# Performance work log

Measured on AMD Instinct MI355X. Metric: run time of the kernel, lower is better.

The kernel has to match this reference:

```python
import jax, jax.numpy as jnp
import numpy as np

EMBED_DIM = 1024
N_HEAD = 16
HEAD_DIM = EMBED_DIM // N_HEAD


def setup_inputs() -> dict:
    key = jax.random.key(0)
    k1, k2, k3 = jax.random.split(key, 3)
    B, S = 2, 2048
    x = jax.random.normal(k1, (B, S, EMBED_DIM), dtype=jnp.float32)
    # kaiming-style scale for the packed QKV projection and output projection
    w_qkv = jax.random.normal(k2, (3 * EMBED_DIM, EMBED_DIM), dtype=jnp.float32) * np.sqrt(2.0 / EMBED_DIM)
    w0 = jax.random.normal(k3, (EMBED_DIM, EMBED_DIM), dtype=jnp.float32) * np.sqrt(2.0 / EMBED_DIM)
    return {"x": x, "w_qkv": w_qkv, "w0": w0}


def reference(x, w_qkv, w0):
    B, S, E = x.shape
    # fused QKV projection (Linear with no bias): x @ w_qkv.T -> [B,S,3E]
    qkv = jnp.einsum('bse,fe->bsf', x, w_qkv)
    q, k, v = jnp.split(qkv, 3, axis=-1)
    # reshape to [B, H, S, D]
    def heads(t):
        return t.reshape(B, S, N_HEAD, HEAD_DIM).transpose(0, 2, 1, 3)
    q, k, v = heads(q), heads(k), heads(v)
    scale = 1.0 / np.sqrt(HEAD_DIM).astype(np.float32)
    scores = jnp.einsum('bhsd,bhtd->bhst', q, k) * scale  # [B,H,S,S]
    # causal additive bias: -inf above the diagonal (same math as the precomputed bias tensor)
    causal = jnp.tril(jnp.ones((S, S), dtype=bool))
    scores = jnp.where(causal, scores, -jnp.inf)
    probs = jax.nn.softmax(scores, axis=-1)
    e = jnp.einsum('bhst,bhtd->bhsd', probs, v)  # [B,H,S,D]
    e = e.transpose(0, 2, 1, 3).reshape(B, S, E)
    # output projection: E @ w0.T
    return jnp.einsum('bse,fe->bsf', e, w0)
```

## Files before the change

### kernel.cpp

```cpp
#include <hip/hip_runtime.h>


typedef unsigned short u16;
typedef short bf16x8 __attribute__((ext_vector_type(8)));
typedef float f32x4 __attribute__((ext_vector_type(4)));
typedef unsigned short u16x4 __attribute__((ext_vector_type(4)));

#define S_LEN 2048
#define EMB 1024
#define NH 16
#define HD 64
#define QKV_W 3072
#define BATCH 2
#define CSC 0.18033688f

static __device__ __forceinline__ u16 f2bf(float f) {
    unsigned x = __float_as_uint(f);
    return (u16)((x + 0x7fffu + ((x >> 16) & 1u)) >> 16);
}

static __device__ __forceinline__ void gld_lds16(const u16* g, u16* l) {
    __builtin_amdgcn_global_load_lds(
        (const __attribute__((address_space(1))) void*)g,
        (__attribute__((address_space(3))) void*)l, 16, 0, 0);
}

#define XN4 (BATCH * S_LEN * EMB / 4)
#define WQ4 (QKV_W * EMB / 4)
#define W04 (EMB * EMB / 4)
__global__ __launch_bounds__(256) void cvt_all(const float* __restrict__ x,
                                               const float* __restrict__ wq,
                                               const float* __restrict__ w0,
                                               u16* __restrict__ xb,
                                               u16* __restrict__ wqb,
                                               u16* __restrict__ w0b) {
    int i = blockIdx.x * 256 + threadIdx.x;
    const float* src;
    u16* dst;
    int off;
    if (i < XN4) { src = x; dst = xb; off = i; }
    else if (i < XN4 + WQ4) { src = wq; dst = wqb; off = i - XN4; }
    else { src = w0; dst = w0b; off = i - XN4 - WQ4; }
    float4 v = ((const float4*)src)[off];
    u16x4 o;
    o[0] = f2bf(v.x); o[1] = f2bf(v.y); o[2] = f2bf(v.z); o[3] = f2bf(v.w);
    ((u16x4*)dst)[off] = o;
}

template <typename OutT, int BN>
__global__ __launch_bounds__(256) void gemm_bt(const u16* __restrict__ A,
                                               const u16* __restrict__ Bt,
                                               OutT* __restrict__ C,
                                               int M, int N, int K, int qcols) {
    constexpr int NF = BN / 32;
    __shared__ alignas(16) u16 As[128 * 32];
    __shared__ alignas(16) u16 Bs[BN * 32];
    const int tid = threadIdx.x;
    const int wave = tid >> 6, lane = tid & 63;
    const int quad = lane >> 4, lr = lane & 15;
    const int m0 = blockIdx.y * 128, n0 = blockIdx.x * BN;
    const int wm = (wave & 1) * 64, wn = (wave >> 1) * (BN / 2);
    const float sc = (n0 < qcols) ? CSC : 1.0f;

    f32x4 acc[4][NF] = {};

    for (int k0 = 0; k0 < K; k0 += 32) {
#pragma unroll
        for (int i = 0; i < 2; ++i) {
            int chunk = tid + i * 256;
            int row = chunk >> 2;
            int col8 = (chunk & 3) * 8;
            gld_lds16(&A[(size_t)(m0 + row) * K + k0 + col8], &As[row * 32 + col8]);
        }
#pragma unroll
        for (int i = 0; i < BN / 64; ++i) {
            int chunk = tid + i * 256;
            int row = chunk >> 2;
            int col8 = (chunk & 3) * 8;
            gld_lds16(&Bt[(size_t)(n0 + row) * K + k0 + col8], &Bs[row * 32 + col8]);
        }
        __syncthreads();
        bf16x8 af[4], bf[NF];
#pragma unroll
        for (int i = 0; i < 4; ++i)
            af[i] = *(const bf16x8*)&As[(wm + i * 16 + lr) * 32 + quad * 8];
#pragma unroll
        for (int i = 0; i < NF; ++i)
            bf[i] = *(const bf16x8*)&Bs[(wn + i * 16 + lr) * 32 + quad * 8];
#pragma unroll
        for (int mi = 0; mi < 4; ++mi)
#pragma unroll
            for (int ni = 0; ni < NF; ++ni)
                acc[mi][ni] = __builtin_amdgcn_mfma_f32_16x16x32_bf16(
                    af[mi], bf[ni], acc[mi][ni], 0, 0, 0);
        __syncthreads();
    }

#pragma unroll
    for (int mi = 0; mi < 4; ++mi) {
#pragma unroll
        for (int r = 0; r < 4; ++r) {
            int gr = m0 + wm + mi * 16 + quad * 4 + r;
#pragma unroll
            for (int ni = 0; ni < NF; ++ni) {
                int gc = n0 + wn + ni * 16 + lr;
                float v = acc[mi][ni][r] * sc;
                if constexpr (sizeof(OutT) == 2)
                    C[(size_t)gr * N + gc] = (OutT)f2bf(v);
                else
                    C[(size_t)gr * N + gc] = (OutT)v;
            }
        }
    }
}

__global__ __launch_bounds__(256) void transpose_v(const u16* __restrict__ qkv,
                                                   u16* __restrict__ vt) {
    __shared__ alignas(16) u16 t[64][72];
    const int s0 = blockIdx.x * 64;
    const int bh = blockIdx.y;
    const int b = bh >> 4, h = bh & 15;
#pragma unroll
    for (int i = 0; i < 2; ++i) {
        int chunk = threadIdx.x + i * 256;
        int row = chunk >> 3;
        int c8 = (chunk & 7) * 8;
        uint4 v = *(const uint4*)&qkv[(size_t)(b * S_LEN + s0 + row) * QKV_W +
                                      2 * EMB + h * HD + c8];
        const u16* p = (const u16*)&v;
#pragma unroll
        for (int jj = 0; jj < 8; ++jj) t[c8 + jj][row] = p[jj];
    }
    __syncthreads();
#pragma unroll
    for (int i = 0; i < 2; ++i) {
        int chunk = threadIdx.x + i * 256;
        int d = chunk >> 3;
        int c8 = (chunk & 7) * 8;
        uint4 v = *(const uint4*)&t[d][c8];
        *(uint4*)&vt[((size_t)bh * HD + d) * S_LEN + s0 + c8] = v;
    }
}

__global__ __launch_bounds__(512, 4) void attn(const u16* __restrict__ qkv,
                                               const u16* __restrict__ vt,
                                               u16* __restrict__ e) {
    const int tid = threadIdx.x;
    const int w = tid >> 6, lane = tid & 63;
    const int quad = lane >> 4, lr = lane & 15;
    const int wq = w & 3, hv = w >> 2;
    const int tA = blockIdx.y;
    const int tB = 31 - tA;
    const int bh = blockIdx.x, b = bh >> 4, h = bh & 15;

    __shared__ alignas(16) u16 smem[17408];
    u16* Ks = smem;
    u16* Vs = smem + 8192;

    const u16* qkv_b = qkv + (size_t)b * S_LEN * QKV_W;
    const u16* qrowA = qkv_b + (size_t)(tA * 64 + wq * 16 + lr) * QKV_W + h * HD + quad * 8;
    const u16* qrowB = qkv_b + (size_t)(tB * 64 + wq * 16 + lr) * QKV_W + h * HD + quad * 8;
    const bf16x8 qfA0 = *(const bf16x8*)(qrowA);
    const bf16x8 qfA1 = *(const bf16x8*)(qrowA + 32);
    const bf16x8 qfB0 = *(const bf16x8*)(qrowB);
    const bf16x8 qfB1 = *(const bf16x8*)(qrowB + 32);

    const u16* kbase = qkv_b + EMB + h * HD;
    const u16* vbase = vt + (size_t)bh * HD * S_LEN;

    f32x4 oA[4] = {}, oB[4] = {};
    float lsA = 0.f, lsB = 0.f;
    const int qgA = tA * 64 + wq * 16 + lr;
    const int qgB = tB * 64 + wq * 16 + lr;

    const int sr = wq * 16 + (lane >> 2);
    const int scl = (lane & 3) * 8;
    const int scg = ((lane & 3) ^ ((lane >> 3) & 3)) * 8;

    auto stage = [&](int j, int bb) {
        const int kv0 = j * 64;
        if (w < 4) {
            gld_lds16(kbase + (size_t)(kv0 + sr) * QKV_W + scg,
                      &Ks[bb * 4096 + sr * 32 + scl]);
            gld_lds16(kbase + (size_t)(kv0 + sr) * QKV_W + 32 + scg,
                      &Ks[bb * 4096 + 2048 + sr * 32 + scl]);
        } else {
            gld_lds16(vbase + (size_t)sr * S_LEN + kv0 + scg,
                      &Vs[bb * 4096 + sr * 32 + scl]);
            gld_lds16(vbase + (size_t)sr * S_LEN + kv0 + 32 + scg,
                      &Vs[bb * 4096 + 2048 + sr * 32 + scl]);
        }
    };

    const int xq8 = (quad ^ ((lr >> 1) & 3)) * 8;

    auto softpack = [&](const f32x4* s, bool diag, int qg, int kvg,
                        float& lsum) -> bf16x8 {
        float p[8];
#pragma unroll
        for (int nt = 0; nt < 2; ++nt)
#pragma unroll
            for (int r = 0; r < 4; ++r) {
                float pv = exp2f(s[nt][r]);
                if (diag) pv = (kvg + nt * 16 + quad * 4 + r > qg) ? 0.f : pv;
                p[nt * 4 + r] = pv;
            }
        lsum += ((p[0] + p[1]) + (p[2] + p[3])) + ((p[4] + p[5]) + (p[6] + p[7]));
        unsigned x0 = __builtin_amdgcn_perm(__float_as_uint(p[1]),
                                            __float_as_uint(p[0]), 0x07060302u);
        unsigned x1 = __builtin_amdgcn_perm(__float_as_uint(p[3]),
                                            __float_as_uint(p[2]), 0x07060302u);
        unsigned x2 = __builtin_amdgcn_perm(__float_as_uint(p[5]),
                                            __float_as_uint(p[4]), 0x07060302u);
        unsigned x3 = __builtin_amdgcn_perm(__float_as_uint(p[7]),
                                            __float_as_uint(p[6]), 0x07060302u);
        asm("v_permlane32_swap_b32 %0, %1" : "+v"(x0), "+v"(x2));
        asm("v_permlane16_swap_b32 %0, %1" : "+v"(x0), "+v"(x2));
        asm("v_permlane32_swap_b32 %0, %1" : "+v"(x1), "+v"(x3));
        asm("v_permlane16_swap_b32 %0, %1" : "+v"(x1), "+v"(x3));
        union { unsigned u[4]; bf16x8 v; } r;
        r.u[0] = x0; r.u[1] = x1; r.u[2] = x2; r.u[3] = x3;
        return r.v;
    };

    stage(0, 0);
    for (int j = 0; j <= tB; ++j) {
        const int bb = j & 1;
        __syncthreads();
        if (j < tB) stage(j + 1, 1 - bb);
        const bool doA = (j <= tA);
        const u16* ks = &Ks[bb * 4096];
        const u16* vs = &Vs[bb * 4096];
        const int kvh = hv * 32;

        f32x4 sB[2], sA[2];
#pragma unroll
        for (int nt = 0; nt < 2; ++nt) {
            const int kvr = kvh + nt * 16 + lr;
            bf16x8 k0 = *(const bf16x8*)&ks[kvr * 32 + xq8];
            bf16x8 k1 = *(const bf16x8*)&ks[2048 + kvr * 32 + xq8];
            f32x4 z = {};
            z = __builtin_amdgcn_mfma_f32_16x16x32_bf16(k0, qfB0, z, 0, 0, 0);
            z = __builtin_amdgcn_mfma_f32_16x16x32_bf16(k1, qfB1, z, 0, 0, 0);
            sB[nt] = z;
            if (doA) {
                f32x4 za = {};
                za = __builtin_amdgcn_mfma_f32_16x16x32_bf16(k0, qfA0, za, 0, 0, 0);
                za = __builtin_amdgcn_mfma_f32_16x16x32_bf16(k1, qfA1, za, 0, 0, 0);
                sA[nt] = za;
            }
        }

        const int kvg = j * 64 + kvh;
        const bf16x8 pB = softpack(sB, j == tB, qgB, kvg, lsB);
        bf16x8 pA = {};
        if (doA) pA = softpack(sA, j == tA, qgA, kvg, lsA);

#pragma unroll
        for (int nt = 0; nt < 4; ++nt) {
            bf16x8 v = *(const bf16x8*)&vs[hv * 2048 + (nt * 16 + lr) * 32 + xq8];
            oB[nt] = __builtin_amdgcn_mfma_f32_16x16x32_bf16(pB, v, oB[nt], 0, 0, 0);
            if (doA) oA[nt] = __builtin_amdgcn_mfma_f32_16x16x32_bf16(pA, v, oA[nt], 0, 0, 0);
        }
    }

    float lfA = lsA + __shfl_xor(lsA, 16, 64);
    lfA += __shfl_xor(lfA, 32, 64);
    float lfB = lsB + __shfl_xor(lsB, 16, 64);
    lfB += __shfl_xor(lfB, 32, 64);
    __syncthreads();
    float* mA = (float*)smem;
    float* mB = mA + 64 * 66;
    float* lAr = mB + 64 * 66;
    float* lBr = lAr + 64;
    if (hv) {
#pragma unroll
        for (int nt = 0; nt < 4; ++nt)
#pragma unroll
            for (int r = 0; r < 4; ++r)
                mA[(wq * 16 + quad * 4 + r) * 66 + nt * 16 + lr] = oA[nt][r];
        if (lane < 16) lAr[wq * 16 + lane] = lfA;
    } else {
#pragma unroll
        for (int nt = 0; nt < 4; ++nt)
#pragma unroll
            for (int r = 0; r < 4; ++r)
                mB[(wq * 16 + quad * 4 + r) * 66 + nt * 16 + lr] = oB[nt][r];
        if (lane < 16) lBr[wq * 16 + lane] = lfB;
    }
    __syncthreads();
    if (!hv) {
        float lff = lfA + lAr[wq * 16 + lr];
#pragma unroll
        for (int r = 0; r < 4; ++r) {
            float inv = 1.0f / __shfl(lff, quad * 4 + r, 64);
            size_t row = (size_t)(b * S_LEN + tA * 64 + wq * 16 + quad * 4 + r) * EMB + h * HD;
#pragma unroll
            for (int nt = 0; nt < 4; ++nt)
                e[row + nt * 16 + lr] =
                    f2bf((oA[nt][r] + mA[(wq * 16 + quad * 4 + r) * 66 + nt * 16 + lr]) * inv);
        }
    } else {
        float lff = lfB + lBr[wq * 16 + lr];
#pragma unroll
        for (int r = 0; r < 4; ++r) {
            float inv = 1.0f / __shfl(lff, quad * 4 + r, 64);
            size_t row = (size_t)(b * S_LEN + tB * 64 + wq * 16 + quad * 4 + r) * EMB + h * HD;
#pragma unroll
            for (int nt = 0; nt < 4; ++nt)
                e[row + nt * 16 + lr] =
                    f2bf((oB[nt][r] + mB[(wq * 16 + quad * 4 + r) * 66 + nt * 16 + lr]) * inv);
        }
    }
}

extern "C" void kernel_launch(void* const* d_in, const int* in_sizes, int n_in,
                              void* d_out, int out_size, void* d_ws, size_t ws_size,
                              hipStream_t stream) {
    const float* x = (const float*)d_in[0];
    const float* w_qkv = (const float*)d_in[1];
    const float* w0 = (const float*)d_in[2];
    float* out = (float*)d_out;

    const size_t M = (size_t)BATCH * S_LEN;
    u16* xb = (u16*)d_ws;
    u16* wqb = xb + M * EMB;
    u16* w0b = wqb + (size_t)QKV_W * EMB;
    u16* qkvb = w0b + (size_t)EMB * EMB;
    u16* vtb = qkvb + M * QKV_W;
    u16* eb = vtb + (size_t)BATCH * NH * HD * S_LEN;

    cvt_all<<<(XN4 + WQ4 + W04) / 256, 256, 0, stream>>>(x, w_qkv, w0, xb, wqb, w0b);

    gemm_bt<u16, 128><<<dim3(QKV_W / 128, M / 128), 256, 0, stream>>>(
        xb, wqb, qkvb, (int)M, QKV_W, EMB, EMB);

    transpose_v<<<dim3(S_LEN / 64, BATCH * NH), 256, 0, stream>>>(qkvb, vtb);

    attn<<<dim3(BATCH * NH, 16), 512, 0, stream>>>(qkvb, vtb, eb);

    gemm_bt<float, 64><<<dim3(EMB / 64, M / 128), 256, 0, stream>>>(
        eb, w0b, out, (int)M, EMB, EMB, 0);
}
```

Measured before the change: 183.7 us.

## Load K and V fragments directly from global into registers, dropping LDS staging

Replaces the double-buffered global-to-LDS staging of K and V tiles (with __syncthreads per KV block) by per-wave direct global loads into MFMA operand registers. K fragments for the next block are prefetched into alternating register sets, and V is loaded after the QK MFMAs so the load overlaps the softmax. It also adds s_setprio around the MFMA sections. This removes the LDS traffic and block barriers, but each wave now fetches its own K/V from global/L2 with no sharing across the four query waves, and global load latency is exposed on a shorter timeline.

```diff
diff --git a/kernel.cpp b/kernel.cpp
--- a/kernel.cpp
+++ b/kernel.cpp
@@ -154,8 +154,6 @@
     const int bh = blockIdx.x, b = bh >> 4, h = bh & 15;
 
     __shared__ alignas(16) u16 smem[17408];
-    u16* Ks = smem;
-    u16* Vs = smem + 8192;
 
     const u16* qkv_b = qkv + (size_t)b * S_LEN * QKV_W;
     const u16* qrowA = qkv_b + (size_t)(tA * 64 + wq * 16 + lr) * QKV_W + h * HD + quad * 8;
@@ -165,34 +163,29 @@
     const bf16x8 qfB0 = *(const bf16x8*)(qrowB);
     const bf16x8 qfB1 = *(const bf16x8*)(qrowB + 32);
 
-    const u16* kbase = qkv_b + EMB + h * HD;
-    const u16* vbase = vt + (size_t)bh * HD * S_LEN;
+    const int kvh = hv * 32;
+    const u16* kbase = qkv_b + EMB + h * HD + (size_t)(kvh + lr) * QKV_W + quad * 8;
+    const u16* vbase = vt + (size_t)bh * HD * S_LEN + (size_t)lr * S_LEN + kvh + quad * 8;
 
     f32x4 oA[4] = {}, oB[4] = {};
     float lsA = 0.f, lsB = 0.f;
     const int qgA = tA * 64 + wq * 16 + lr;
     const int qgB = tB * 64 + wq * 16 + lr;
 
-    const int sr = wq * 16 + (lane >> 2);
-    const int scl = (lane & 3) * 8;
-    const int scg = ((lane & 3) ^ ((lane >> 3) & 3)) * 8;
-
-    auto stage = [&](int j, int bb) {
-        const int kv0 = j * 64;
-        if (w < 4) {
-            gld_lds16(kbase + (size_t)(kv0 + sr) * QKV_W + scg,
-                      &Ks[bb * 4096 + sr * 32 + scl]);
-            gld_lds16(kbase + (size_t)(kv0 + sr) * QKV_W + 32 + scg,
-                      &Ks[bb * 4096 + 2048 + sr * 32 + scl]);
-        } else {
-            gld_lds16(vbase + (size_t)sr * S_LEN + kv0 + scg,
-                      &Vs[bb * 4096 + sr * 32 + scl]);
-            gld_lds16(vbase + (size_t)sr * S_LEN + kv0 + 32 + scg,
-                      &Vs[bb * 4096 + 2048 + sr * 32 + scl]);
+    auto loadK = [&](int j, bf16x8 (&kf)[4]) {
+        const u16* kp = kbase + (size_t)j * 64 * QKV_W;
+#pragma unroll
+        for (int nt = 0; nt < 2; ++nt) {
+            kf[2 * nt]     = *(const bf16x8*)(kp + (size_t)nt * 16 * QKV_W);
+            kf[2 * nt + 1] = *(const bf16x8*)(kp + (size_t)nt * 16 * QKV_W + 32);
         }
     };
-
-    const int xq8 = (quad ^ ((lr >> 1) & 3)) * 8;
+    auto loadV = [&](int j, bf16x8 (&vf)[4]) {
+        const u16* vp = vbase + j * 64;
+#pragma unroll
+        for (int nt = 0; nt < 4; ++nt)
+            vf[nt] = *(const bf16x8*)(vp + (size_t)nt * 16 * S_LEN);
+    };
 
     auto softpack = [&](const f32x4* s, bool diag, int qg, int kvg,
                         float& lsum) -> bf16x8 {
@@ -223,45 +216,47 @@
         return r.v;
     };
 
-    stage(0, 0);
-    for (int j = 0; j <= tB; ++j) {
-        const int bb = j & 1;
-        __syncthreads();
-        if (j < tB) stage(j + 1, 1 - bb);
+    auto iterate = [&](int j, bf16x8 (&kv)[4]) {
         const bool doA = (j <= tA);
-        const u16* ks = &Ks[bb * 4096];
-        const u16* vs = &Vs[bb * 4096];
-        const int kvh = hv * 32;
-
         f32x4 sB[2], sA[2];
+        __builtin_amdgcn_s_setprio(1);
 #pragma unroll
         for (int nt = 0; nt < 2; ++nt) {
-            const int kvr = kvh + nt * 16 + lr;
-            bf16x8 k0 = *(const bf16x8*)&ks[kvr * 32 + xq8];
-            bf16x8 k1 = *(const bf16x8*)&ks[2048 + kvr * 32 + xq8];
             f32x4 z = {};
-            z = __builtin_amdgcn_mfma_f32_16x16x32_bf16(k0, qfB0, z, 0, 0, 0);
-            z = __builtin_amdgcn_mfma_f32_16x16x32_bf16(k1, qfB1, z, 0, 0, 0);
+            z = __builtin_amdgcn_mfma_f32_16x16x32_bf16(kv[2 * nt], qfB0, z, 0, 0, 0);
+            z = __builtin_amdgcn_mfma_f32_16x16x32_bf16(kv[2 * nt + 1], qfB1, z, 0, 0, 0);
             sB[nt] = z;
             if (doA) {
                 f32x4 za = {};
-                za = __builtin_amdgcn_mfma_f32_16x16x32_bf16(k0, qfA0, za, 0, 0, 0);
-                za = __builtin_amdgcn_mfma_f32_16x16x32_bf16(k1, qfA1, za, 0, 0, 0);
+                za = __builtin_amdgcn_mfma_f32_16x16x32_bf16(kv[2 * nt], qfA0, za, 0, 0, 0);
+                za = __builtin_amdgcn_mfma_f32_16x16x32_bf16(kv[2 * nt + 1], qfA1, za, 0, 0, 0);
                 sA[nt] = za;
             }
         }
-
+        __builtin_amdgcn_s_setprio(0);
+        loadV(j, kv);
         const int kvg = j * 64 + kvh;
         const bf16x8 pB = softpack(sB, j == tB, qgB, kvg, lsB);
         bf16x8 pA = {};
         if (doA) pA = softpack(sA, j == tA, qgA, kvg, lsA);
-
+        __builtin_amdgcn_s_setprio(1);
 #pragma unroll
         for (int nt = 0; nt < 4; ++nt) {
-            bf16x8 v = *(const bf16x8*)&vs[hv * 2048 + (nt * 16 + lr) * 32 + xq8];
-            oB[nt] = __builtin_amdgcn_mfma_f32_16x16x32_bf16(pB, v, oB[nt], 0, 0, 0);
-            if (doA) oA[nt] = __builtin_amdgcn_mfma_f32_16x16x32_bf16(pA, v, oA[nt], 0, 0, 0);
-        }
+            oB[nt] = __builtin_amdgcn_mfma_f32_16x16x32_bf16(pB, kv[nt], oB[nt], 0, 0, 0);
+            if (doA)
+                oA[nt] = __builtin_amdgcn_mfma_f32_16x16x32_bf16(pA, kv[nt], oA[nt], 0, 0, 0);
+        }
+        __builtin_amdgcn_s_setprio(0);
+    };
+
+    bf16x8 kvX[4], kvY[4];
+    loadK(0, kvX);
+    for (int j = 0; j <= tB; j += 2) {
+        if (j < tB) loadK(j + 1, kvY);
+        iterate(j, kvX);
+        if (j + 1 > tB) break;
+        if (j + 1 < tB) loadK(j + 2, kvX);
+        iterate(j + 1, kvY);
     }
 
     float lfA = lsA + __shfl_xor(lsA, 16, 64);
```

Result: slower. 245.7 us (+33.7%).

## Halve attention block to 4 waves, each computing two 16-row query fragments

Applied to the files above, without the earlier changes.

The attention kernel now uses 256 threads (4 waves) instead of 512. Each wave handles two 16-row query fragments, so every K and V fragment read from LDS feeds twice as many MFMAs. All four waves now stage both K and V tiles, and the tile-pair order across blockIdx.y is permuted so that long and short causal work interleaves. The cost is higher register use per wave (launch bounds drop to 2 blocks) and fewer waves available to hide latency.

```diff
diff --git a/kernel.cpp b/kernel.cpp
--- a/kernel.cpp
+++ b/kernel.cpp
@@ -142,14 +142,15 @@
     }
 }
 
-__global__ __launch_bounds__(512, 4) void attn(const u16* __restrict__ qkv,
+__global__ __launch_bounds__(256, 2) void attn(const u16* __restrict__ qkv,
                                                const u16* __restrict__ vt,
                                                u16* __restrict__ e) {
     const int tid = threadIdx.x;
     const int w = tid >> 6, lane = tid & 63;
     const int quad = lane >> 4, lr = lane & 15;
-    const int wq = w & 3, hv = w >> 2;
-    const int tA = blockIdx.y;
+    const int g = w & 1, hv = w >> 1;
+    const int y = blockIdx.y;
+    const int tA = (y < 8) ? y : 23 - y;
     const int tB = 31 - tA;
     const int bh = blockIdx.x, b = bh >> 4, h = bh & 15;
 
@@ -158,38 +159,40 @@
     u16* Vs = smem + 8192;
 
     const u16* qkv_b = qkv + (size_t)b * S_LEN * QKV_W;
-    const u16* qrowA = qkv_b + (size_t)(tA * 64 + wq * 16 + lr) * QKV_W + h * HD + quad * 8;
-    const u16* qrowB = qkv_b + (size_t)(tB * 64 + wq * 16 + lr) * QKV_W + h * HD + quad * 8;
-    const bf16x8 qfA0 = *(const bf16x8*)(qrowA);
-    const bf16x8 qfA1 = *(const bf16x8*)(qrowA + 32);
-    const bf16x8 qfB0 = *(const bf16x8*)(qrowB);
-    const bf16x8 qfB1 = *(const bf16x8*)(qrowB + 32);
+    bf16x8 qfA[2][2], qfB[2][2];
+    int qgA[2], qgB[2];
+#pragma unroll
+    for (int f = 0; f < 2; ++f) {
+        const u16* qra = qkv_b + (size_t)(tA * 64 + g * 32 + f * 16 + lr) * QKV_W + h * HD + quad * 8;
+        const u16* qrb = qkv_b + (size_t)(tB * 64 + g * 32 + f * 16 + lr) * QKV_W + h * HD + quad * 8;
+        qfA[f][0] = *(const bf16x8*)qra;
+        qfA[f][1] = *(const bf16x8*)(qra + 32);
+        qfB[f][0] = *(const bf16x8*)qrb;
+        qfB[f][1] = *(const bf16x8*)(qrb + 32);
+        qgA[f] = tA * 64 + g * 32 + f * 16 + lr;
+        qgB[f] = tB * 64 + g * 32 + f * 16 + lr;
+    }
 
     const u16* kbase = qkv_b + EMB + h * HD;
     const u16* vbase = vt + (size_t)bh * HD * S_LEN;
 
-    f32x4 oA[4] = {}, oB[4] = {};
-    float lsA = 0.f, lsB = 0.f;
-    const int qgA = tA * 64 + wq * 16 + lr;
-    const int qgB = tB * 64 + wq * 16 + lr;
-
-    const int sr = wq * 16 + (lane >> 2);
+    f32x4 oA[2][4] = {}, oB[2][4] = {};
+    float lsA[2] = {0.f, 0.f}, lsB[2] = {0.f, 0.f};
+
+    const int sr = w * 16 + (lane >> 2);
     const int scl = (lane & 3) * 8;
     const int scg = ((lane & 3) ^ ((lane >> 3) & 3)) * 8;
 
     auto stage = [&](int j, int bb) {
         const int kv0 = j * 64;
-        if (w < 4) {
-            gld_lds16(kbase + (size_t)(kv0 + sr) * QKV_W + scg,
-                      &Ks[bb * 4096 + sr * 32 + scl]);
-            gld_lds16(kbase + (size_t)(kv0 + sr) * QKV_W + 32 + scg,
-                      &Ks[bb * 4096 + 2048 + sr * 32 + scl]);
-        } else {
-            gld_lds16(vbase + (size_t)sr * S_LEN + kv0 + scg,
-                      &Vs[bb * 4096 + sr * 32 + scl]);
-            gld_lds16(vbase + (size_t)sr * S_LEN + kv0 + 32 + scg,
-                      &Vs[bb * 4096 + 2048 + sr * 32 + scl]);
-        }
+        gld_lds16(kbase + (size_t)(kv0 + sr) * QKV_W + scg,
+                  &Ks[bb * 4096 + sr * 32 + scl]);
+        gld_lds16(kbase + (size_t)(kv0 + sr) * QKV_W + 32 + scg,
+                  &Ks[bb * 4096 + 2048 + sr * 32 + scl]);
+        gld_lds16(vbase + (size_t)sr * S_LEN + kv0 + scg,
+                  &Vs[bb * 4096 + sr * 32 + scl]);
+        gld_lds16(vbase + (size_t)sr * S_LEN + kv0 + 32 + scg,
+                  &Vs[bb * 4096 + 2048 + sr * 32 + scl]);
     };
 
     const int xq8 = (quad ^ ((lr >> 1) & 3)) * 8;
@@ -233,41 +236,60 @@
         const u16* vs = &Vs[bb * 4096];
         const int kvh = hv * 32;
 
-        f32x4 sB[2], sA[2];
+        bf16x8 k0[2], k1[2];
 #pragma unroll
         for (int nt = 0; nt < 2; ++nt) {
             const int kvr = kvh + nt * 16 + lr;
-            bf16x8 k0 = *(const bf16x8*)&ks[kvr * 32 + xq8];
-            bf16x8 k1 = *(const bf16x8*)&ks[2048 + kvr * 32 + xq8];
-            f32x4 z = {};
-            z = __builtin_amdgcn_mfma_f32_16x16x32_bf16(k0, qfB0, z, 0, 0, 0);
-            z = __builtin_amdgcn_mfma_f32_16x16x32_bf16(k1, qfB1, z, 0, 0, 0);
-            sB[nt] = z;
-            if (doA) {
-                f32x4 za = {};
-                za = __builtin_amdgcn_mfma_f32_16x16x32_bf16(k0, qfA0, za, 0, 0, 0);
-                za = __builtin_amdgcn_mfma_f32_16x16x32_bf16(k1, qfA1, za, 0, 0, 0);
-                sA[nt] = za;
-            }
-        }
+            k0[nt] = *(const bf16x8*)&ks[kvr * 32 + xq8];
+            k1[nt] = *(const bf16x8*)&ks[2048 + kvr * 32 + xq8];
+        }
+        f32x4 sB[2][2], sA[2][2];
+#pragma unroll
+        for (int f = 0; f < 2; ++f)
+#pragma unroll
+            for (int nt = 0; nt < 2; ++nt) {
+                f32x4 z = {};
+                z = __builtin_amdgcn_mfma_f32_16x16x32_bf16(k0[nt], qfB[f][0], z, 0, 0, 0);
+                z = __builtin_amdgcn_mfma_f32_16x16x32_bf16(k1[nt], qfB[f][1], z, 0, 0, 0);
+                sB[f][nt] = z;
+                if (doA) {
+                    f32x4 za = {};
+                    za = __builtin_amdgcn_mfma_f32_16x16x32_bf16(k0[nt], qfA[f][0], za, 0, 0, 0);
+                    za = __builtin_amdgcn_mfma_f32_16x16x32_bf16(k1[nt], qfA[f][1], za, 0, 0, 0);
+                    sA[f][nt] = za;
+                }
+            }
 
         const int kvg = j * 64 + kvh;
-        const bf16x8 pB = softpack(sB, j == tB, qgB, kvg, lsB);
-        bf16x8 pA = {};
-        if (doA) pA = softpack(sA, j == tA, qgA, kvg, lsA);
+        bf16x8 pB[2], pA[2];
+#pragma unroll
+        for (int f = 0; f < 2; ++f)
+            pB[f] = softpack(sB[f], j == tB, qgB[f], kvg, lsB[f]);
+        if (doA)
+#pragma unroll
+            for (int f = 0; f < 2; ++f)
+                pA[f] = softpack(sA[f], j == tA, qgA[f], kvg, lsA[f]);
 
 #pragma unroll
         for (int nt = 0; nt < 4; ++nt) {
             bf16x8 v = *(const bf16x8*)&vs[hv * 2048 + (nt * 16 + lr) * 32 + xq8];
-            oB[nt] = __builtin_amdgcn_mfma_f32_16x16x32_bf16(pB, v, oB[nt], 0, 0, 0);
-            if (doA) oA[nt] = __builtin_amdgcn_mfma_f32_16x16x32_bf16(pA, v, oA[nt], 0, 0, 0);
-        }
-    }
-
-    float lfA = lsA + __shfl_xor(lsA, 16, 64);
-    lfA += __shfl_xor(lfA, 32, 64);
-    float lfB = lsB + __shfl_xor(lsB, 16, 64);
-    lfB += __shfl_xor(lfB, 32, 64);
+#pragma unroll
+            for (int f = 0; f < 2; ++f) {
+                oB[f][nt] = __builtin_amdgcn_mfma_f32_16x16x32_bf16(pB[f], v, oB[f][nt], 0, 0, 0);
+                if (doA)
+                    oA[f][nt] = __builtin_amdgcn_mfma_f32_16x16x32_bf16(pA[f], v, oA[f][nt], 0, 0, 0);
+            }
+        }
+    }
+
+    float lfA[2], lfB[2];
+#pragma unroll
+    for (int f = 0; f < 2; ++f) {
+        lfA[f] = lsA[f] + __shfl_xor(lsA[f], 16, 64);
+        lfA[f] += __shfl_xor(lfA[f], 32, 64);
+        lfB[f] = lsB[f] + __shfl_xor(lsB[f], 16, 64);
+        lfB[f] += __shfl_xor(lfB[f], 32, 64);
+    }
     __syncthreads();
     float* mA = (float*)smem;
     float* mB = mA + 64 * 66;
@@ -275,41 +297,53 @@
     float* lBr = lAr + 64;
     if (hv) {
 #pragma unroll
-        for (int nt = 0; nt < 4; ++nt)
-#pragma unroll
-            for (int r = 0; r < 4; ++r)
-                mA[(wq * 16 + quad * 4 + r) * 66 + nt * 16 + lr] = oA[nt][r];
-        if (lane < 16) lAr[wq * 16 + lane] = lfA;
+        for (int f = 0; f < 2; ++f) {
+#pragma unroll
+            for (int nt = 0; nt < 4; ++nt)
+#pragma unroll
+                for (int r = 0; r < 4; ++r)
+                    mA[(g * 32 + f * 16 + quad * 4 + r) * 66 + nt * 16 + lr] = oA[f][nt][r];
+            if (lane < 16) lAr[g * 32 + f * 16 + lane] = lfA[f];
+        }
     } else {
 #pragma unroll
-        for (int nt = 0; nt < 4; ++nt)
-#pragma unroll
-            for (int r = 0; r < 4; ++r)
-                mB[(wq * 16 + quad * 4 + r) * 66 + nt * 16 + lr] = oB[nt][r];
-        if (lane < 16) lBr[wq * 16 + lane] = lfB;
+        for (int f = 0; f < 2; ++f) {
+#pragma unroll
+            for (int nt = 0; nt < 4; ++nt)
+#pragma unroll
+                for (int r = 0; r < 4; ++r)
+                    mB[(g * 32 + f * 16 + quad * 4 + r) * 66 + nt * 16 + lr] = oB[f][nt][r];
+            if (lane < 16) lBr[g * 32 + f * 16 + lane] = lfB[f];
+        }
     }
     __syncthreads();
     if (!hv) {
-        float lff = lfA + lAr[wq * 16 + lr];
-#pragma unroll
-        for (int r = 0; r < 4; ++r) {
-            float inv = 1.0f / __shfl(lff, quad * 4 + r, 64);
-            size_t row = (size_t)(b * S_LEN + tA * 64 + wq * 16 + quad * 4 + r) * EMB + h * HD;
-#pragma unroll
-            for (int nt = 0; nt < 4; ++nt)
-                e[row + nt * 16 + lr] =
-                    f2bf((oA[nt][r] + mA[(wq * 16 + quad * 4 + r) * 66 + nt * 16 + lr]) * inv);
+#pragma unroll
+        for (int f = 0; f < 2; ++f) {
+            float lff = lfA[f] + lAr[g * 32 + f * 16 + lr];
+#pragma unroll
+            for (int r = 0; r < 4; ++r) {
+                float inv = 1.0f / __shfl(lff, quad * 4 + r, 64);
+                size_t row = (size_t)(b * S_LEN + tA * 64 + g * 32 + f * 16 + quad * 4 + r) * EMB + h * HD;
+#pragma unroll
+                for (int nt = 0; nt < 4; ++nt)
+                    e[row + nt * 16 + lr] =
+                        f2bf((oA[f][nt][r] + mA[(g * 32 + f * 16 + quad * 4 + r) * 66 + nt * 16 + lr]) * inv);
+            }
         }
     } else {
-        float lff = lfB + lBr[wq * 16 + lr];
-#pragma unroll
-        for (int r = 0; r < 4; ++r) {
-            float inv = 1.0f / __shfl(lff, quad * 4 + r, 64);
-            size_t row = (size_t)(b * S_LEN + tB * 64 + wq * 16 + quad * 4 + r) * EMB + h * HD;
-#pragma unroll
-            for (int nt = 0; nt < 4; ++nt)
-                e[row + nt * 16 + lr] =
-                    f2bf((oB[nt][r] + mB[(wq * 16 + quad * 4 + r) * 66 + nt * 16 + lr]) * inv);
+#pragma unroll
+        for (int f = 0; f < 2; ++f) {
+            float lff = lfB[f] + lBr[g * 32 + f * 16 + lr];
+#pragma unroll
+            for (int r = 0; r < 4; ++r) {
+                float inv = 1.0f / __shfl(lff, quad * 4 + r, 64);
+                size_t row = (size_t)(b * S_LEN + tB * 64 + g * 32 + f * 16 + quad * 4 + r) * EMB + h * HD;
+#pragma unroll
+                for (int nt = 0; nt < 4; ++nt)
+                    e[row + nt * 16 + lr] =
+                        f2bf((oB[f][nt][r] + mB[(g * 32 + f * 16 + quad * 4 + r) * 66 + nt * 16 + lr]) * inv);
+            }
         }
     }
 }
@@ -337,7 +371,7 @@
 
     transpose_v<<<dim3(S_LEN / 64, BATCH * NH), 256, 0, stream>>>(qkvb, vtb);
 
-    attn<<<dim3(BATCH * NH, 16), 512, 0, stream>>>(qkvb, vtb, eb);
+    attn<<<dim3(BATCH * NH, 16), 256, 0, stream>>>(qkvb, vtb, eb);
 
     gemm_bt<float, 64><<<dim3(EMB / 64, M / 128), 256, 0, stream>>>(
         eb, w0b, out, (int)M, EMB, EMB, 0);
```

Measured after the change: 183.9 us. About the same (+0.1%).
